# Optimization experiments

Hardware: AMD Instinct MI355X
Metric: run time of the kernel (lower is better)

Reference implementation:

```python
import jax, jax.numpy as jnp
import numpy as np

N_NODES = 50000
N_DIRECTED = 800000  # symmetrized to 1.6M (src,dst) pairs
IN_FEAT = 256
HEADS = 8
OUT = 64


def setup_inputs() -> dict:
    key = jax.random.key(0)
    k1, k2, k3, k4, k5 = jax.random.split(key, 5)
    r = jax.random.randint(k1, (N_DIRECTED,), 0, N_NODES)
    c = jax.random.randint(k2, (N_DIRECTED,), 0, N_NODES)
    # symmetric adjacency (values = 1), as edge list
    src = jnp.concatenate([r, c])
    dst = jnp.concatenate([c, r])
    x = jax.random.normal(k3, (N_NODES, IN_FEAT), dtype=jnp.float32)
    Ws = jax.random.normal(k4, (HEADS, OUT, IN_FEAT), dtype=jnp.float32) * 0.05
    As = jax.random.normal(k5, (HEADS, 2 * OUT, 1), dtype=jnp.float32) * 0.05
    return {"x": x, "src": src, "dst": dst, "Ws": Ws, "As": As}


def reference(x, src, dst, Ws, As):
    H, O, F = Ws.shape
    N = x.shape[0]
    # t_nodes = inputs @ Ws^T  -> [H, N, O]
    t = jnp.einsum('nf,hof->hno', x, Ws)
    a_l = As[:, :O, 0]   # [H, O]
    a_r = As[:, O:, 0]   # [H, O]
    Al = jnp.einsum('hno,ho->hn', t, a_l)  # [H, N]
    Ar = jnp.einsum('hno,ho->hn', t, a_r)  # [H, N]
    outs = []
    for k in range(H):
        # sparse E[i,j] = Al[i] + Ar[j] on adjacency pattern
        e = Al[k][src] + Ar[k][dst]  # [E]
        # NOTE: original applies tf.sparse.softmax to E directly (its lrelu
        # tensor is computed but never used), so no leaky_relu here.
        m = jax.ops.segment_max(e, src, num_segments=N)
        ex = jnp.exp(e - m[src])
        den = jax.ops.segment_sum(ex, src, num_segments=N)
        alpha = ex / den[src]
        # sparse_dense_matmul(alphas, t_nodes[k])
        h = jax.ops.segment_sum(alpha[:, None] * t[k][dst], src, num_segments=N)
        outs.append(h)
    out = jnp.stack(outs, axis=1)          # [N, H, O]
    out = out.reshape(N, H * O)            # reduction=False -> concat heads
    return jax.nn.elu(out)
```

## Files before the change

### kernel.cpp

```cpp
#include <hip/hip_runtime.h>
#include <hip/hip_bf16.h>

#define NN 50000
#define INF 256
#define NH 8
#define OUTF 64
#define NC 512
#define NTILES 782
#define EPB 8192
#define NBK 391
#define NBX 12501

typedef __attribute__((ext_vector_type(8))) short bf16x8;
typedef __attribute__((ext_vector_type(4))) float f32x4;
typedef __attribute__((ext_vector_type(2))) float v2f;
typedef __attribute__((ext_vector_type(8))) float f32x8;

__device__ __forceinline__ unsigned short f2bf(float f){
  unsigned u = __float_as_uint(f);
  u += 0x7FFFu + ((u>>16)&1u);
  return (unsigned short)(u>>16);
}

#define GLOAD_LDS16(g, s) \
  __builtin_amdgcn_global_load_lds((const __attribute__((address_space(1))) void*)(g), \
                                   (__attribute__((address_space(3))) void*)(s), 16, 0, 0)

__global__ void k_atil(const float* __restrict__ W, const float* __restrict__ As,
                       float* __restrict__ atil){
  const int h = blockIdx.x, f = threadIdx.x;
  float s = 0.f;
  for (int o=0;o<64;o++) s += W[((long)h*64+o)*INF + f] * As[h*128 + 64 + o];
  atil[h*256 + f] = s;
}

__global__ __launch_bounds__(256) void k_front(const float* __restrict__ x,
                                               const float* __restrict__ W,
                                               unsigned short* __restrict__ Wt,
                                               const float* __restrict__ atil,
                                               unsigned short* __restrict__ xb,
                                               float* __restrict__ eAr,
                                               const int* __restrict__ src,
                                               int* __restrict__ M,
                                               int E, int NB){
  __shared__ int hh[NBK];
  const int tid = threadIdx.x;
  const int bid = blockIdx.x;
  if (bid < 8){
    const int r = tid>>2, cb = (tid&3)*64;
    char* tile = (char*)(Wt + (size_t)bid*16384);
    const float* Wr = W + ((long)bid*64 + r)*INF;
#pragma unroll
    for (int i=0;i<16;i++){
      int c = cb + i*4;
      float4 v = *(const float4*)(Wr + c);
      ushort4 b; b.x=f2bf(v.x); b.y=f2bf(v.y); b.z=f2bf(v.z); b.w=f2bf(v.w);
      int addr = r*512 + ((((c>>3) ^ (r&7)))<<4) + ((c&7)<<1);
      *(ushort4*)(tile + addr) = b;
    }
    return;
  }
  if (bid < 8+NB){
    const int b = bid-8;
    for (int i=tid;i<NBK;i+=256) hh[i]=0;
    __syncthreads();
    const int base = b*EPB;
    const int lim = min(E-base, EPB);
    for (int i=tid;i<lim;i+=256) atomicAdd(&hh[src[base+i]>>7], 1);
    __syncthreads();
    for (int i=tid;i<NBK;i+=256) M[(long)i*NB + b] = hh[i];
    return;
  }
  const int w = tid>>6, l = tid&63;
  const long n = (long)(bid-8-NB)*4 + w;
  if (n > NN) return;
  if (n == NN){
    uint2 z; z.x=0; z.y=0;
    *(uint2*)((char*)xb + (size_t)n*512 + l*8) = z;
    if (l < 8) eAr[n*NH + l] = 0.f;
    return;
  }
  float4 v = *(const float4*)(x + n*INF + l*4);
  uint2 d;
  d.x = (unsigned)f2bf(v.x) | ((unsigned)f2bf(v.y)<<16);
  d.y = (unsigned)f2bf(v.z) | ((unsigned)f2bf(v.w)<<16);
  *(uint2*)((char*)xb + (size_t)n*512 + l*8) = d;
  float p[8];
#pragma unroll
  for (int h=0;h<8;h++){
    float4 a = *(const float4*)(atil + h*256 + l*4);
    p[h] = v.x*a.x + v.y*a.y + v.z*a.z + v.w*a.w;
  }
#pragma unroll
  for (int off=1; off<64; off<<=1){
#pragma unroll
    for (int h=0;h<8;h++) p[h] += __shfl_xor(p[h], off, 64);
  }
  if (l < 8){
    float e = p[0];
#pragma unroll
    for (int h=1;h<8;h++) if (l==h) e = p[h];
    eAr[n*NH + l] = __expf(e);
  }
}

__global__ __launch_bounds__(256) void k_bscan(int* __restrict__ M,
                                               int* __restrict__ tot, int NB){
  __shared__ int lds[256];
  const int k = blockIdx.x, tid = threadIdx.x;
  int v = (tid<NB) ? M[(long)k*NB+tid] : 0;
  const int orig = v;
  lds[tid]=v; __syncthreads();
  for (int off=1; off<256; off<<=1){
    int a = (tid>=off)? lds[tid-off] : 0;
    __syncthreads(); lds[tid]+=a; __syncthreads();
  }
  if (tid<NB) M[(long)k*NB+tid] = lds[tid]-orig;
  if (tid==255) tot[k] = lds[255];
}

__global__ __launch_bounds__(512) void k_sscan(const int* __restrict__ in,
                                               int* __restrict__ out, int n){
  __shared__ int lds[512];
  const int tid = threadIdx.x;
  int v = (tid<n)? in[tid] : 0;
  const int orig = v;
  lds[tid]=v; __syncthreads();
  for (int off=1; off<512; off<<=1){
    int a = (tid>=off)? lds[tid-off] : 0;
    __syncthreads(); lds[tid]+=a; __syncthreads();
  }
  if (tid<=n) out[tid] = lds[tid]-orig;
}

__global__ __launch_bounds__(256) void k_bscat(const int* __restrict__ src,
                                               const int* __restrict__ dst,
                                               const int* __restrict__ M,
                                               const int* __restrict__ bOff,
                                               unsigned* __restrict__ ebuf,
                                               int E, int NB){
  __shared__ int cur[NBK];
  const int tid = threadIdx.x, b = blockIdx.x;
  for (int i=tid;i<NBK;i+=256) cur[i] = bOff[i] + M[(long)i*NB + b];
  __syncthreads();
  const int base = b*EPB;
  const int lim = min(E-base, EPB);
  for (int i=tid;i<lim;i+=256){
    int s = src[base+i], d = dst[base+i];
    int p = atomicAdd(&cur[s>>7], 1);
    ebuf[p] = ((unsigned)d<<7) | (unsigned)(s&127);
  }
}

__global__ __launch_bounds__(256) void k_bcnt2(const unsigned* __restrict__ ebuf,
                                               const int* __restrict__ bOff,
                                               int* __restrict__ cnt,
                                               int* __restrict__ pbTot){
  __shared__ int h[128];
  __shared__ int ps[128];
  const int k = blockIdx.x, tid = threadIdx.x;
  if (tid<128) h[tid]=0;
  __syncthreads();
  const int beg = bOff[k], end = bOff[k+1];
  for (int i=beg+tid; i<end; i+=256)
    atomicAdd(&h[(int)(ebuf[i] & 127u)], 1);
  __syncthreads();
  if (tid<128){
    cnt[(k<<7)+tid] = h[tid];
    ps[tid] = (h[tid]+7)&~7;
  }
  __syncthreads();
  for (int off=64; off>0; off>>=1){
    if (tid<off) ps[tid] += ps[tid+off];
    __syncthreads();
  }
  if (tid==0) pbTot[k] = ps[0];
}

__global__ __launch_bounds__(256) void k_final(const unsigned* __restrict__ ebuf,
                                               const int* __restrict__ bOff,
                                               const int* __restrict__ cnt,
                                               const int* __restrict__ pbOff,
                                               int* __restrict__ row_ptr,
                                               int* __restrict__ col){
  __shared__ int s[128];
  __shared__ int cur[128];
  __shared__ int pend[128];
  const int k = blockIdx.x, tid = threadIdx.x;
  int c = 0, pc = 0;
  if (tid<128){
    c = cnt[(k<<7)+tid];
    pc = (c+7)&~7;
    s[tid] = pc;
  }
  __syncthreads();
  for (int off=1; off<128; off<<=1){
    int a = (tid>=off && tid<128)? s[tid-off] : 0;
    __syncthreads();
    if (tid<128) s[tid] += a;
    __syncthreads();
  }
  const int base = pbOff[k];
  if (tid<128){
    int rp = base + s[tid] - pc;
    row_ptr[(k<<7)+tid] = rp;
    cur[tid] = rp;
    pend[tid] = rp + pc;
  }
  __syncthreads();
  const int beg = bOff[k], end = bOff[k+1];
  for (int i=beg+tid; i<end; i+=256){
    unsigned e = ebuf[i];
    int p = atomicAdd(&cur[e & 127u], 1);
    col[p] = (int)(e>>7);
  }
  __syncthreads();
  if (tid<128){
    for (int i=cur[tid]; i<pend[tid]; i++) col[i] = NN;
  }
}

__global__ __launch_bounds__(256) void k_aggr2(const int* __restrict__ row_ptr,
                                               const int* __restrict__ col,
                                               const unsigned short* __restrict__ xb,
                                               const float* __restrict__ eAr,
                                               unsigned short* __restrict__ g,
                                               float* __restrict__ den,
                                               int tile0){
  const int tid = threadIdx.x, l = tid&63;
  const int wv = tid>>6;
  const int fh = wv&1;
  const long n = (long)tile0*64 + blockIdx.x*2 + (wv>>1);
  if (n >= NN) return;
  const int beg = __builtin_amdgcn_readfirstlane(row_ptr[n]);
  const int end = __builtin_amdgcn_readfirstlane(row_ptr[n+1]);
  const char* xbp = (const char*)xb + fh*256;
  v2f acc[8] = {};
  float dnl = 0.f;
  const long l4 = (long)l*4;
  const int lw = l&7;

  for (int i=beg; i<end; i+=8){
    int cc[8];
#pragma unroll
    for (int e=0;e<8;e++) cc[e] = __builtin_amdgcn_readfirstlane(col[i+e]);
    unsigned q[8];
#pragma unroll
    for (int e=0;e<8;e++) q[e] = *(const unsigned*)(xbp + (size_t)cc[e]*512 + l4);
    float wl[8];
#pragma unroll
    for (int e=0;e<8;e++) wl[e] = eAr[(size_t)cc[e]*NH + lw];
#pragma unroll
    for (int e=0;e<8;e++) dnl += wl[e];
#pragma unroll
    for (int e=0;e<8;e++){
      f32x8 wv8 = *(const f32x8*)(eAr + (size_t)cc[e]*NH);
      v2f f01;
      f01.x = __uint_as_float(q[e]<<16);
      f01.y = __uint_as_float(q[e]&0xffff0000u);
#pragma unroll
      for (int h=0;h<8;h++){
        v2f w2; w2.x = wv8[h]; w2.y = wv8[h];
        acc[h] = __builtin_elementwise_fma(w2, f01, acc[h]);
      }
    }
  }

  const int lt = (int)(n>>6) - tile0;
  const int r  = (int)(n&63);
  char* tb = (char*)g + (size_t)lt*262144 + r*512 + fh*256 + l*4;
#pragma unroll
  for (int h=0;h<8;h++){
    unsigned d = (unsigned)f2bf(acc[h].x) | ((unsigned)f2bf(acc[h].y)<<16);
    *(unsigned*)(tb + h*32768) = d;
  }
  if (fh==0 && l < 8) den[n*NH + l] = dnl;
}

__global__ __launch_bounds__(256) void k_gemm2(const unsigned short* __restrict__ g,
                                               const unsigned short* __restrict__ Wt,
                                               const float* __restrict__ den,
                                               float* __restrict__ out,
                                               int tile0){
  __shared__ unsigned short As[16384];
  __shared__ unsigned short Bs[16384];
  __shared__ float linv[64];
  const int tid = threadIdx.x, w = tid>>6, l = tid&63;
  const int brow = tile0 + blockIdx.x;
  const int h = blockIdx.y;
  {
    const char* gb = (const char*)g + (size_t)blockIdx.x*262144 + h*32768;
    char* dstA = (char*)As + w*8192;
#pragma unroll
    for (int k=0;k<8;k++){
      int r = w*16 + k*2 + (l>>5);
      const char* sA = gb + r*512 + (((l&31) ^ (r&7))<<4);
      GLOAD_LDS16(sA, dstA + k*1024);
    }
    const char* srcB = (const char*)Wt + (size_t)h*32768 + w*8192 + l*16;
    char* dstB = (char*)Bs + w*8192;
#pragma unroll
    for (int k=0;k<8;k++) GLOAD_LDS16(srcB + k*1024, dstB + k*1024);
  }
  if (tid < 64){
    long gr = (long)brow*64 + tid;
    float dv = (gr < NN) ? den[gr*NH + h] : 1.f;
    linv[tid] = dv > 0.f ? 1.f/dv : 0.f;
  }
  asm volatile("s_waitcnt vmcnt(0)");
  __syncthreads();

  const int col = w*16 + (l&15);
  f32x4 acc[4] = {};
#pragma unroll
  for (int ks=0; ks<8; ks++){
    int chunkB = (ks*4 + (l>>4)) ^ (col&7);
    bf16x8 bfrag = *(const bf16x8*)((char*)Bs + col*512 + (chunkB<<4));
#pragma unroll
    for (int mt=0; mt<4; mt++){
      int ar_ = mt*16 + (l&15);
      int chunkA = (ks*4 + (l>>4)) ^ (ar_&7);
      bf16x8 afrag = *(const bf16x8*)((char*)As + ar_*512 + (chunkA<<4));
      acc[mt] = __builtin_amdgcn_mfma_f32_16x16x32_bf16(afrag, bfrag, acc[mt], 0,0,0);
    }
  }
#pragma unroll
  for (int mt=0; mt<4; mt++){
#pragma unroll
    for (int j=0;j<4;j++){
      int r = mt*16 + (l>>4)*4 + j;
      long gr = (long)brow*64 + r;
      if (gr < NN){
        float v = acc[mt][j] * linv[r];
        out[gr*NC + h*64 + col] = v>0.f ? v : expm1f(v);
      }
    }
  }
}

extern "C" void kernel_launch(void* const* d_in, const int* in_sizes, int n_in,
                              void* d_out, int out_size, void* d_ws, size_t ws_size,
                              hipStream_t stream){
  const float* x   = (const float*)d_in[0];
  const int*   src = (const int*)d_in[1];
  const int*   dst = (const int*)d_in[2];
  const float* Ws  = (const float*)d_in[3];
  const float* Av  = (const float*)d_in[4];
  const int E = in_sizes[1];
  const int NB = (E + EPB - 1) / EPB;

  char* ws = (char*)d_ws;
  size_t off = 0;
  auto alloc = [&](size_t bytes)->void*{
    void* p = ws + off; off += (bytes + 255) & ~(size_t)255; return p;
  };
  unsigned short* xb   = (unsigned short*)alloc((size_t)50048*512);
  float* eAr           = (float*)alloc((size_t)50048*NH*4);
  float* atil          = (float*)alloc(8*256*4);
  float* den           = (float*)alloc((size_t)50048*NH*4);
  unsigned short* Wt   = (unsigned short*)alloc((size_t)8*32768);
  int*   cnt           = (int*)alloc(50304*4);
  int*   row_ptr       = (int*)alloc(50304*4);
  int*   M             = (int*)alloc((size_t)NBK*256*4);
  int*   tot           = (int*)alloc(512*4);
  int*   bOff          = (int*)alloc(512*4);
  int*   pbTot         = (int*)alloc(512*4);
  int*   pbOff         = (int*)alloc(512*4);
  int*   col           = (int*)alloc(((size_t)E + 8*50048 + 64)*4);

  size_t remain = (ws_size > off + 256) ? (ws_size - off - 256) : 0;
  int chunk = (int)(remain / 262144);
  if (chunk > NTILES) chunk = NTILES;
  if (chunk < 25) chunk = 25;
  unsigned short* g = (unsigned short*)alloc((size_t)chunk*262144);
  unsigned* ebuf = (unsigned*)g;

  k_atil<<<8,256,0,stream>>>(Ws, Av, atil);
  k_front<<<8+NB+NBX,256,0,stream>>>(x, Ws, Wt, atil, xb, eAr, src, M, E, NB);
  k_bscan<<<NBK,256,0,stream>>>(M, tot, NB);
  k_sscan<<<1,512,0,stream>>>(tot, bOff, NBK);
  k_bscat<<<NB,256,0,stream>>>(src, dst, M, bOff, ebuf, E, NB);
  k_bcnt2<<<NBK,256,0,stream>>>(ebuf, bOff, cnt, pbTot);
  k_sscan<<<1,512,0,stream>>>(pbTot, pbOff, NBK);
  k_final<<<NBK,256,0,stream>>>(ebuf, bOff, cnt, pbOff, row_ptr, col);

  int tile0 = 0;
  while (tile0 < NTILES){
    int tiles = NTILES - tile0 < chunk ? NTILES - tile0 : chunk;
    k_aggr2<<<tiles*32,256,0,stream>>>(row_ptr, col, xb, eAr, g, den, tile0);
    k_gemm2<<<dim3(tiles,8),256,0,stream>>>(g, Wt, den, (float*)d_out, tile0);
    tile0 += tiles;
  }
}
```

Before: 310.4 us.

## Replace single-block scans with atomic cursor allocation and fuse count/final kernels

Result: no change. 312.3 us (+0.6%).

```diff
diff --git a/kernel.cpp b/kernel.cpp
--- a/kernel.cpp
+++ b/kernel.cpp
@@ -27,8 +27,9 @@
                                    (__attribute__((address_space(3))) void*)(s), 16, 0, 0)
 
 __global__ void k_atil(const float* __restrict__ W, const float* __restrict__ As,
-                       float* __restrict__ atil){
+                       float* __restrict__ atil, int* __restrict__ cursor){
   const int h = blockIdx.x, f = threadIdx.x;
+  if (h==0 && f==0){ cursor[0]=0; cursor[1]=0; }
   float s = 0.f;
   for (int o=0;o<64;o++) s += W[((long)h*64+o)*INF + f] * As[h*128 + 64 + o];
   atil[h*256 + f] = s;
@@ -105,8 +106,11 @@
 }
 
 __global__ __launch_bounds__(256) void k_bscan(int* __restrict__ M,
-                                               int* __restrict__ tot, int NB){
+                                               int* __restrict__ bOff,
+                                               int* __restrict__ bEnd,
+                                               int* __restrict__ cursor, int NB){
   __shared__ int lds[256];
+  __shared__ int sb;
   const int k = blockIdx.x, tid = threadIdx.x;
   int v = (tid<NB) ? M[(long)k*NB+tid] : 0;
   const int orig = v;
@@ -115,33 +119,25 @@
     int a = (tid>=off)? lds[tid-off] : 0;
     __syncthreads(); lds[tid]+=a; __syncthreads();
   }
-  if (tid<NB) M[(long)k*NB+tid] = lds[tid]-orig;
-  if (tid==255) tot[k] = lds[255];
-}
-
-__global__ __launch_bounds__(512) void k_sscan(const int* __restrict__ in,
-                                               int* __restrict__ out, int n){
-  __shared__ int lds[512];
-  const int tid = threadIdx.x;
-  int v = (tid<n)? in[tid] : 0;
-  const int orig = v;
-  lds[tid]=v; __syncthreads();
-  for (int off=1; off<512; off<<=1){
-    int a = (tid>=off)? lds[tid-off] : 0;
-    __syncthreads(); lds[tid]+=a; __syncthreads();
-  }
-  if (tid<=n) out[tid] = lds[tid]-orig;
+  if (tid==255){
+    int tot = lds[255];
+    int base = atomicAdd(&cursor[0], tot);
+    sb = base;
+    bOff[k] = base;
+    bEnd[k] = base + tot;
+  }
+  __syncthreads();
+  if (tid<NB) M[(long)k*NB+tid] = sb + lds[tid]-orig;
 }
 
 __global__ __launch_bounds__(256) void k_bscat(const int* __restrict__ src,
                                                const int* __restrict__ dst,
                                                const int* __restrict__ M,
-                                               const int* __restrict__ bOff,
                                                unsigned* __restrict__ ebuf,
                                                int E, int NB){
   __shared__ int cur[NBK];
   const int tid = threadIdx.x, b = blockIdx.x;
-  for (int i=tid;i<NBK;i+=256) cur[i] = bOff[i] + M[(long)i*NB + b];
+  for (int i=tid;i<NBK;i+=256) cur[i] = M[(long)i*NB + b];
   __syncthreads();
   const int base = b*EPB;
   const int lim = min(E-base, EPB);
@@ -152,45 +148,28 @@
   }
 }
 
-__global__ __launch_bounds__(256) void k_bcnt2(const unsigned* __restrict__ ebuf,
-                                               const int* __restrict__ bOff,
-                                               int* __restrict__ cnt,
-                                               int* __restrict__ pbTot){
+__global__ __launch_bounds__(256) void k_bcnt_final(const unsigned* __restrict__ ebuf,
+                                                    const int* __restrict__ bOff,
+                                                    const int* __restrict__ bEnd,
+                                                    int* __restrict__ rbeg,
+                                                    int* __restrict__ rend,
+                                                    int* __restrict__ col,
+                                                    int* __restrict__ cursor){
   __shared__ int h[128];
-  __shared__ int ps[128];
-  const int k = blockIdx.x, tid = threadIdx.x;
-  if (tid<128) h[tid]=0;
-  __syncthreads();
-  const int beg = bOff[k], end = bOff[k+1];
-  for (int i=beg+tid; i<end; i+=256)
-    atomicAdd(&h[(int)(ebuf[i] & 127u)], 1);
-  __syncthreads();
-  if (tid<128){
-    cnt[(k<<7)+tid] = h[tid];
-    ps[tid] = (h[tid]+7)&~7;
-  }
-  __syncthreads();
-  for (int off=64; off>0; off>>=1){
-    if (tid<off) ps[tid] += ps[tid+off];
-    __syncthreads();
-  }
-  if (tid==0) pbTot[k] = ps[0];
-}
-
-__global__ __launch_bounds__(256) void k_final(const unsigned* __restrict__ ebuf,
-                                               const int* __restrict__ bOff,
-                                               const int* __restrict__ cnt,
-                                               const int* __restrict__ pbOff,
-                                               int* __restrict__ row_ptr,
-                                               int* __restrict__ col){
   __shared__ int s[128];
   __shared__ int cur[128];
   __shared__ int pend[128];
+  __shared__ int sb;
   const int k = blockIdx.x, tid = threadIdx.x;
-  int c = 0, pc = 0;
+  if (tid<128) h[tid]=0;
+  __syncthreads();
+  const int beg = bOff[k], end = bEnd[k];
+  for (int i=beg+tid; i<end; i+=256)
+    atomicAdd(&h[(int)(ebuf[i] & 127u)], 1);
+  __syncthreads();
+  int pc = 0;
   if (tid<128){
-    c = cnt[(k<<7)+tid];
-    pc = (c+7)&~7;
+    pc = (h[tid]+7)&~7;
     s[tid] = pc;
   }
   __syncthreads();
@@ -200,15 +179,18 @@
     if (tid<128) s[tid] += a;
     __syncthreads();
   }
-  const int base = pbOff[k];
+  if (tid==0){
+    sb = atomicAdd(&cursor[1], s[127]);
+  }
+  __syncthreads();
   if (tid<128){
-    int rp = base + s[tid] - pc;
-    row_ptr[(k<<7)+tid] = rp;
+    int rp = sb + s[tid] - pc;
+    rbeg[(k<<7)+tid] = rp;
+    rend[(k<<7)+tid] = rp + pc;
     cur[tid] = rp;
     pend[tid] = rp + pc;
   }
   __syncthreads();
-  const int beg = bOff[k], end = bOff[k+1];
   for (int i=beg+tid; i<end; i+=256){
     unsigned e = ebuf[i];
     int p = atomicAdd(&cur[e & 127u], 1);
@@ -220,7 +202,8 @@
   }
 }
 
-__global__ __launch_bounds__(256) void k_aggr2(const int* __restrict__ row_ptr,
+__global__ __launch_bounds__(256) void k_aggr2(const int* __restrict__ rbeg,
+                                               const int* __restrict__ rend,
                                                const int* __restrict__ col,
                                                const unsigned short* __restrict__ xb,
                                                const float* __restrict__ eAr,
@@ -232,8 +215,8 @@
   const int fh = wv&1;
   const long n = (long)tile0*64 + blockIdx.x*2 + (wv>>1);
   if (n >= NN) return;
-  const int beg = __builtin_amdgcn_readfirstlane(row_ptr[n]);
-  const int end = __builtin_amdgcn_readfirstlane(row_ptr[n+1]);
+  const int beg = __builtin_amdgcn_readfirstlane(rbeg[n]);
+  const int end = __builtin_amdgcn_readfirstlane(rend[n]);
   const char* xbp = (const char*)xb + fh*256;
   v2f acc[8] = {};
   float dnl = 0.f;
@@ -359,13 +342,12 @@
   float* atil          = (float*)alloc(8*256*4);
   float* den           = (float*)alloc((size_t)50048*NH*4);
   unsigned short* Wt   = (unsigned short*)alloc((size_t)8*32768);
-  int*   cnt           = (int*)alloc(50304*4);
-  int*   row_ptr       = (int*)alloc(50304*4);
+  int*   rbeg          = (int*)alloc(50304*4);
+  int*   rend          = (int*)alloc(50304*4);
   int*   M             = (int*)alloc((size_t)NBK*256*4);
-  int*   tot           = (int*)alloc(512*4);
   int*   bOff          = (int*)alloc(512*4);
-  int*   pbTot         = (int*)alloc(512*4);
-  int*   pbOff         = (int*)alloc(512*4);
+  int*   bEnd          = (int*)alloc(512*4);
+  int*   cursor        = (int*)alloc(256);
   int*   col           = (int*)alloc(((size_t)E + 8*50048 + 64)*4);
 
   size_t remain = (ws_size > off + 256) ? (ws_size - off - 256) : 0;
@@ -375,19 +357,16 @@
   unsigned short* g = (unsigned short*)alloc((size_t)chunk*262144);
   unsigned* ebuf = (unsigned*)g;
 
-  k_atil<<<8,256,0,stream>>>(Ws, Av, atil);
+  k_atil<<<8,256,0,stream>>>(Ws, Av, atil, cursor);
   k_front<<<8+NB+NBX,256,0,stream>>>(x, Ws, Wt, atil, xb, eAr, src, M, E, NB);
-  k_bscan<<<NBK,256,0,stream>>>(M, tot, NB);
-  k_sscan<<<1,512,0,stream>>>(tot, bOff, NBK);
-  k_bscat<<<NB,256,0,stream>>>(src, dst, M, bOff, ebuf, E, NB);
-  k_bcnt2<<<NBK,256,0,stream>>>(ebuf, bOff, cnt, pbTot);
-  k_sscan<<<1,512,0,stream>>>(pbTot, pbOff, NBK);
-  k_final<<<NBK,256,0,stream>>>(ebuf, bOff, cnt, pbOff, row_ptr, col);
+  k_bscan<<<NBK,256,0,stream>>>(M, bOff, bEnd, cursor, NB);
+  k_bscat<<<NB,256,0,stream>>>(src, dst, M, ebuf, E, NB);
+  k_bcnt_final<<<NBK,256,0,stream>>>(ebuf, bOff, bEnd, rbeg, rend, col, cursor);
 
   int tile0 = 0;
   while (tile0 < NTILES){
     int tiles = NTILES - tile0 < chunk ? NTILES - tile0 : chunk;
-    k_aggr2<<<tiles*32,256,0,stream>>>(row_ptr, col, xb, eAr, g, den, tile0);
+    k_aggr2<<<tiles*32,256,0,stream>>>(rbeg, rend, col, xb, eAr, g, den, tile0);
     k_gemm2<<<dim3(tiles,8),256,0,stream>>>(g, Wt, den, (float*)d_out, tile0);
     tile0 += tiles;
   }
```
